# Kernel tuning notes

Hardware: AMD Instinct MI355X
Metric: run time of the kernel (lower is better)

The kernel has to match this reference:

```python
import jax, jax.numpy as jnp
import numpy as np

NEG_INF = -1e6

def setup_inputs() -> dict:
    key = jax.random.key(0)
    ks = jax.random.split(key, 7)
    B, Q, K, D, H = 16, 64, 1024, 256, 128
    return {
        "queries": jax.random.normal(ks[0], (B, Q, D), dtype=jnp.float32),
        "keys": jax.random.normal(ks[1], (B, K, D), dtype=jnp.float32),
        "values": jax.random.normal(ks[2], (B, K, D), dtype=jnp.float32),
        "valid_lens": jax.random.randint(ks[3], (B,), 1, K + 1, dtype=jnp.int32),
        "W_q": jax.random.normal(ks[4], (D, H), dtype=jnp.float32) * (1.0 / np.sqrt(D)),
        "W_k": jax.random.normal(ks[5], (D, H), dtype=jnp.float32) * (1.0 / np.sqrt(D)),
        "w_v": jax.random.normal(ks[6], (H,), dtype=jnp.float32) * (1.0 / np.sqrt(H)),
    }

def reference(queries, keys, values, valid_lens, W_q, W_k, w_v):
    # project: [B,Q,H], [B,K,H]
    q = jnp.einsum('bqd,dh->bqh', queries, W_q)
    k = jnp.einsum('bkd,dh->bkh', keys, W_k)
    # broadcast add -> tanh -> score: [B,Q,K]
    features = jnp.tanh(q[:, :, None, :] + k[:, None, :, :])  # [B,Q,K,H]
    scores = jnp.einsum('bqkh,h->bqk', features, w_v)
    # masked softmax over key axis (valid_lens per batch)
    K_len = keys.shape[1]
    mask = jnp.arange(K_len)[None, None, :] < valid_lens[:, None, None]  # [B,1,K]
    scores = jnp.where(mask, scores, NEG_INF)
    attn = jax.nn.softmax(scores, axis=-1)
    # weighted sum of values: [B,Q,Dv]  (dropout p=0 -> identity)
    return jnp.einsum('bqk,bkd->bqd', attn, values)
```

## Files before the change

### kernel.cpp

```cpp
#include <hip/hip_runtime.h>

#define DDIM 256
#define HDIM 128
#define KLEN 1024
#define SCL 2.8853900817779268f

__global__ __launch_bounds__(256) void proj_kernel(
    const float* __restrict__ queries, const float* __restrict__ keys,
    const float* __restrict__ W_q, const float* __restrict__ W_k,
    float* __restrict__ Eq, float* __restrict__ Ek)
{
    __shared__ union {
        float a[64 * 64];
        float t[32][68];
    } sm;

    const int tid  = threadIdx.x;
    const int lane = tid & 63;
    const int wav  = tid >> 6;

    int blk = blockIdx.x;
    bool iskey; int b = 0, kc0 = 0, hb, row0;
    const float* in; const float* W;
    if (blk < 1024) {
        iskey = true;
        int xcd = blk & 7, s = blk >> 3;
        b = ((s >> 6) << 3) | xcd;
        int r6 = s & 63;
        kc0 = (r6 >> 2) << 6;
        hb  = (r6 & 3) << 5;
        row0 = b * KLEN + kc0;
        in = keys; W = W_k;
    } else {
        iskey = false;
        int qrb = blk - 1024;
        row0 = (qrb >> 2) << 6;
        hb   = (qrb & 3) << 5;
        in = queries; W = W_q;
    }

    const int hg8 = __builtin_amdgcn_readfirstlane(wav << 3);
    const float* Wu = W + hb + hg8;

    const int srow = tid >> 4;
    const int sgd  = tid & 15;
    const float* gsrc = in + (size_t)(row0 + srow) * DDIM + (sgd << 2);

    float4 pf0 = *(const float4*)(gsrc);
    float4 pf1 = *(const float4*)(gsrc + 16 * DDIM);
    float4 pf2 = *(const float4*)(gsrc + 32 * DDIM);
    float4 pf3 = *(const float4*)(gsrc + 48 * DDIM);

    float acc[8];
    #pragma unroll
    for (int c = 0; c < 8; c++) acc[c] = 0.f;

    const int w0 = (srow)      * 64 + ((sgd ^ ((srow)      & 7)) << 2);
    const int w1 = (srow + 16) * 64 + ((sgd ^ ((srow + 16) & 7)) << 2);
    const int w2 = (srow + 32) * 64 + ((sgd ^ ((srow + 32) & 7)) << 2);
    const int w3 = (srow + 48) * 64 + ((sgd ^ ((srow + 48) & 7)) << 2);

    for (int dt0 = 0; dt0 < DDIM; dt0 += 64) {
        *(float4*)(sm.a + w0) = pf0;
        *(float4*)(sm.a + w1) = pf1;
        *(float4*)(sm.a + w2) = pf2;
        *(float4*)(sm.a + w3) = pf3;
        __syncthreads();
        if (dt0 < DDIM - 64) {
            const float* g2 = gsrc + dt0 + 64;
            pf0 = *(const float4*)(g2);
            pf1 = *(const float4*)(g2 + 16 * DDIM);
            pf2 = *(const float4*)(g2 + 32 * DDIM);
            pf3 = *(const float4*)(g2 + 48 * DDIM);
        }
        const float* arow = sm.a + lane * 64;
        const int lx = lane & 7;
        #pragma unroll
        for (int d4 = 0; d4 < 64; d4 += 4) {
            float4 a = *(const float4*)(arow + ((((d4 >> 2)) ^ lx) << 2));
            const float* wr = Wu + (size_t)(dt0 + d4) * HDIM;
            #pragma unroll
            for (int c = 0; c < 8; c++) acc[c] = fmaf(a.x, wr[c],            acc[c]);
            #pragma unroll
            for (int c = 0; c < 8; c++) acc[c] = fmaf(a.y, wr[HDIM + c],     acc[c]);
            #pragma unroll
            for (int c = 0; c < 8; c++) acc[c] = fmaf(a.z, wr[2 * HDIM + c], acc[c]);
            #pragma unroll
            for (int c = 0; c < 8; c++) acc[c] = fmaf(a.w, wr[3 * HDIM + c], acc[c]);
        }
        __syncthreads();
    }

    float e[8];
    #pragma unroll
    for (int c = 0; c < 8; c++) e[c] = __builtin_amdgcn_exp2f(SCL * acc[c]);

    if (!iskey) {
        float* dst = Eq + (size_t)(row0 + lane) * HDIM + hb + hg8;
        *(float4*)(dst)     = make_float4(e[0], e[1], e[2], e[3]);
        *(float4*)(dst + 4) = make_float4(e[4], e[5], e[6], e[7]);
    } else {
        #pragma unroll
        for (int c = 0; c < 8; c++) sm.t[(wav << 3) + c][lane] = e[c];
        __syncthreads();
        float* dstb = Ek + (size_t)b * HDIM * KLEN + (size_t)hb * KLEN + kc0;
        #pragma unroll
        for (int i = 0; i < 2; i++) {
            int g = tid + (i << 8);
            int h = g >> 4, k4 = (g & 15) << 2;
            float4 o = *(const float4*)(&sm.t[h][k4]);
            *(float4*)(dstb + (size_t)h * KLEN + k4) = o;
        }
    }
}

__global__ __launch_bounds__(512) void score_kernel(
    const float* __restrict__ Eq, const float* __restrict__ Ek,
    const float* __restrict__ w_v, const int* __restrict__ valid_lens,
    float* __restrict__ p)
{
    __shared__ float4 eqw[HDIM];
    __shared__ float red0[8], red1[8];

    int tid = threadIdx.x, lane = tid & 63, wav = tid >> 6;
    int blk = blockIdx.x;
    int xcd = blk & 7, s = blk >> 3;
    int b = ((s >= 32) ? 8 : 0) + xcd;
    int qp = s & 31;
    int bq0 = b * 64 + qp * 2;
    int vlen = valid_lens[b];

    if (tid < HDIM) {
        float w2 = -2.0f * w_v[tid];
        eqw[tid] = make_float4(Eq[(size_t)bq0 * HDIM + tid],
                               Eq[(size_t)(bq0 + 1) * HDIM + tid], w2, 0.f);
    }
    __syncthreads();

    int k0 = tid << 1;
    float s00 = -1e30f, s01 = -1e30f, s10 = -1e30f, s11 = -1e30f;
    if (k0 < vlen) {
        const float* ekp = Ek + (size_t)b * HDIM * KLEN + k0;
        float a00 = 0.f, a01 = 0.f, a10 = 0.f, a11 = 0.f;
        #pragma unroll 4
        for (int h = 0; h < HDIM; h++) {
            float2 ek = *(const float2*)(ekp + (size_t)h * KLEN);
            float4 e  = eqw[h];
            a00 = fmaf(e.z, __builtin_amdgcn_rcpf(fmaf(e.x, ek.x, 1.f)), a00);
            a01 = fmaf(e.z, __builtin_amdgcn_rcpf(fmaf(e.x, ek.y, 1.f)), a01);
            a10 = fmaf(e.z, __builtin_amdgcn_rcpf(fmaf(e.y, ek.x, 1.f)), a10);
            a11 = fmaf(e.z, __builtin_amdgcn_rcpf(fmaf(e.y, ek.y, 1.f)), a11);
        }
        s00 = a00; s10 = a10;
        if (k0 + 1 < vlen) { s01 = a01; s11 = a11; }
    }

    float m0 = fmaxf(s00, s01), m1 = fmaxf(s10, s11);
    #pragma unroll
    for (int off = 32; off > 0; off >>= 1) {
        m0 = fmaxf(m0, __shfl_xor(m0, off, 64));
        m1 = fmaxf(m1, __shfl_xor(m1, off, 64));
    }
    if (lane == 0) { red0[wav] = m0; red1[wav] = m1; }
    __syncthreads();
    m0 = red0[0]; m1 = red1[0];
    #pragma unroll
    for (int i = 1; i < 8; i++) {
        m0 = fmaxf(m0, red0[i]);
        m1 = fmaxf(m1, red1[i]);
    }

    float e00 = __expf(s00 - m0), e01 = __expf(s01 - m0);
    float e10 = __expf(s10 - m1), e11 = __expf(s11 - m1);
    float t0 = e00 + e01, t1 = e10 + e11;
    #pragma unroll
    for (int off = 32; off > 0; off >>= 1) {
        t0 += __shfl_xor(t0, off, 64);
        t1 += __shfl_xor(t1, off, 64);
    }
    __syncthreads();
    if (lane == 0) { red0[wav] = t0; red1[wav] = t1; }
    __syncthreads();
    t0 = red0[0]; t1 = red1[0];
    #pragma unroll
    for (int i = 1; i < 8; i++) { t0 += red0[i]; t1 += red1[i]; }
    float inv0 = 1.0f / t0, inv1 = 1.0f / t1;

    float* p0 = p + (size_t)bq0 * KLEN + k0;
    *(float2*)(p0)        = make_float2(e00 * inv0, e01 * inv0);
    *(float2*)(p0 + KLEN) = make_float2(e10 * inv1, e11 * inv1);
}

__global__ __launch_bounds__(256) void av_kernel(
    const float* __restrict__ p, const float* __restrict__ values,
    const int* __restrict__ valid_lens, float* __restrict__ part)
{
    __shared__ float pt[128][10];

    int blk = blockIdx.x;
    int xcd = blk & 7, s = blk >> 3;
    int b = ((s >> 6) << 3) | xcd;
    int r = s & 63, qt = r >> 3, kq = r & 7;
    int tid = threadIdx.x, lane = tid & 63, w = tid >> 6;
    int vlen = valid_lens[b];
    int kbeg = kq << 7;
    int kc = vlen - kbeg; kc = kc < 0 ? 0 : (kc > 128 ? 128 : kc);
    int kc4 = (kc + 3) & ~3;
    int bq0 = b * 64 + qt * 8;

    {
        int q = tid >> 5, k4 = (tid & 31) << 2;
        float4 pv = *(const float4*)(p + (size_t)(bq0 + q) * KLEN + kbeg + k4);
        pt[k4 + 0][q] = pv.x;
        pt[k4 + 1][q] = pv.y;
        pt[k4 + 2][q] = pv.z;
        pt[k4 + 3][q] = pv.w;
    }
    __syncthreads();

    const float* vb = values + ((size_t)b * KLEN + kbeg) * DDIM + (lane << 2);
    float4 a0 = make_float4(0.f, 0.f, 0.f, 0.f);
    float4 a1 = make_float4(0.f, 0.f, 0.f, 0.f);

    for (int k = 0; k < kc4; k += 4) {
        #pragma unroll
        for (int i = 0; i < 4; i++) {
            float2 pp = *(const float2*)(&pt[k + i][w << 1]);
            float4 v  = *(const float4*)(vb + (size_t)(k + i) * DDIM);
            a0.x = fmaf(pp.x, v.x, a0.x); a0.y = fmaf(pp.x, v.y, a0.y);
            a0.z = fmaf(pp.x, v.z, a0.z); a0.w = fmaf(pp.x, v.w, a0.w);
            a1.x = fmaf(pp.y, v.x, a1.x); a1.y = fmaf(pp.y, v.y, a1.y);
            a1.z = fmaf(pp.y, v.z, a1.z); a1.w = fmaf(pp.y, v.w, a1.w);
        }
    }
    float* d0 = part + ((size_t)kq * 1024 + bq0 + (w << 1)) * DDIM + (lane << 2);
    *(float4*)(d0)        = a0;
    *(float4*)(d0 + DDIM) = a1;
}

__global__ __launch_bounds__(256) void combine_kernel(
    const float* __restrict__ part, float* __restrict__ out)
{
    int i = blockIdx.x * 256 + threadIdx.x;
    const float4* p4 = (const float4*)part;
    float4 a = p4[i];
    #pragma unroll
    for (int j = 1; j < 8; j++) {
        float4 v = p4[(size_t)j * 65536 + i];
        a.x += v.x; a.y += v.y; a.z += v.z; a.w += v.w;
    }
    ((float4*)out)[i] = a;
}

extern "C" void kernel_launch(void* const* d_in, const int* in_sizes, int n_in,
                              void* d_out, int out_size, void* d_ws, size_t ws_size,
                              hipStream_t stream) {
    const float* queries    = (const float*)d_in[0];
    const float* keys       = (const float*)d_in[1];
    const float* values     = (const float*)d_in[2];
    const int*   valid_lens = (const int*)d_in[3];
    const float* W_q        = (const float*)d_in[4];
    const float* W_k        = (const float*)d_in[5];
    const float* w_v        = (const float*)d_in[6];

    float* Eq   = (float*)d_ws;
    float* Ek   = Eq + 131072;
    float* p    = Ek + 2097152;
    float* part = Ek;

    proj_kernel<<<1088, 256, 0, stream>>>(queries, keys, W_q, W_k, Eq, Ek);
    score_kernel<<<512, 512, 0, stream>>>(Eq, Ek, w_v, valid_lens, p);
    av_kernel<<<1024, 256, 0, stream>>>(p, values, valid_lens, part);
    combine_kernel<<<256, 256, 0, stream>>>(part, (float*)d_out);
}
```

Measured before the change: 147.5 us.

## Restructure AV kernel so each thread accumulates all eight queries with in-block k reduction

The attention-times-values kernel now has each wave cover a 128-key slice and accumulate all 8 queries of the tile per thread. Each value load is therefore reused across 8 queries instead of 2, and the four waves' partials are reduced in shared memory. The split over keys drops from 8 chunks to 2, so the partial buffer and the combine kernel read a quarter as much data. The grid shrinks to 256 blocks and each thread holds 32 accumulator registers, which may lower occupancy and parallelism on this GPU.

```diff
diff --git a/kernel.cpp b/kernel.cpp
--- a/kernel.cpp
+++ b/kernel.cpp
@@ -195,47 +195,74 @@
     const float* __restrict__ p, const float* __restrict__ values,
     const int* __restrict__ valid_lens, float* __restrict__ part)
 {
-    __shared__ float pt[128][10];
+    __shared__ union {
+        float  pt[512][8];
+        float4 slab[4][8][64];
+    } sm;
 
     int blk = blockIdx.x;
     int xcd = blk & 7, s = blk >> 3;
-    int b = ((s >> 6) << 3) | xcd;
-    int r = s & 63, qt = r >> 3, kq = r & 7;
+    int b = ((s >> 4) << 3) | xcd;
+    int r = s & 15, qt = r >> 1, kh = r & 1;
     int tid = threadIdx.x, lane = tid & 63, w = tid >> 6;
     int vlen = valid_lens[b];
-    int kbeg = kq << 7;
-    int kc = vlen - kbeg; kc = kc < 0 ? 0 : (kc > 128 ? 128 : kc);
-    int kc4 = (kc + 3) & ~3;
     int bq0 = b * 64 + qt * 8;
-
-    {
-        int q = tid >> 5, k4 = (tid & 31) << 2;
-        float4 pv = *(const float4*)(p + (size_t)(bq0 + q) * KLEN + kbeg + k4);
-        pt[k4 + 0][q] = pv.x;
-        pt[k4 + 1][q] = pv.y;
-        pt[k4 + 2][q] = pv.z;
-        pt[k4 + 3][q] = pv.w;
-    }
-    __syncthreads();
-
-    const float* vb = values + ((size_t)b * KLEN + kbeg) * DDIM + (lane << 2);
-    float4 a0 = make_float4(0.f, 0.f, 0.f, 0.f);
-    float4 a1 = make_float4(0.f, 0.f, 0.f, 0.f);
-
-    for (int k = 0; k < kc4; k += 4) {
-        #pragma unroll
-        for (int i = 0; i < 4; i++) {
-            float2 pp = *(const float2*)(&pt[k + i][w << 1]);
-            float4 v  = *(const float4*)(vb + (size_t)(k + i) * DDIM);
-            a0.x = fmaf(pp.x, v.x, a0.x); a0.y = fmaf(pp.x, v.y, a0.y);
-            a0.z = fmaf(pp.x, v.z, a0.z); a0.w = fmaf(pp.x, v.w, a0.w);
-            a1.x = fmaf(pp.y, v.x, a1.x); a1.y = fmaf(pp.y, v.y, a1.y);
-            a1.z = fmaf(pp.y, v.z, a1.z); a1.w = fmaf(pp.y, v.w, a1.w);
-        }
-    }
-    float* d0 = part + ((size_t)kq * 1024 + bq0 + (w << 1)) * DDIM + (lane << 2);
-    *(float4*)(d0)        = a0;
-    *(float4*)(d0 + DDIM) = a1;
+    int kbase = kh << 9;
+
+    #pragma unroll
+    for (int i = 0; i < 4; i++) {
+        int slot = tid + (i << 8);
+        int q = slot >> 7, k4 = (slot & 127) << 2;
+        float4 pv = *(const float4*)(p + (size_t)(bq0 + q) * KLEN + kbase + k4);
+        sm.pt[k4 + 0][q] = pv.x;
+        sm.pt[k4 + 1][q] = pv.y;
+        sm.pt[k4 + 2][q] = pv.z;
+        sm.pt[k4 + 3][q] = pv.w;
+    }
+    __syncthreads();
+
+    int kw = w << 7;
+    int cnt = vlen - (kbase + kw); cnt = cnt < 0 ? 0 : (cnt > 128 ? 128 : cnt);
+    int cnt4 = (cnt + 3) & ~3;
+    const float* vb = values + ((size_t)b * KLEN + kbase + kw) * DDIM + (lane << 2);
+
+    float4 acc[8];
+    #pragma unroll
+    for (int q = 0; q < 8; q++) acc[q] = make_float4(0.f, 0.f, 0.f, 0.f);
+
+    for (int k = 0; k < cnt4; k += 4) {
+        #pragma unroll
+        for (int j = 0; j < 4; j++) {
+            float4 v  = *(const float4*)(vb + (size_t)(k + j) * DDIM);
+            float4 p0 = *(const float4*)(&sm.pt[kw + k + j][0]);
+            float4 p1 = *(const float4*)(&sm.pt[kw + k + j][4]);
+            float pq[8] = {p0.x, p0.y, p0.z, p0.w, p1.x, p1.y, p1.z, p1.w};
+            #pragma unroll
+            for (int q = 0; q < 8; q++) {
+                acc[q].x = fmaf(pq[q], v.x, acc[q].x);
+                acc[q].y = fmaf(pq[q], v.y, acc[q].y);
+                acc[q].z = fmaf(pq[q], v.z, acc[q].z);
+                acc[q].w = fmaf(pq[q], v.w, acc[q].w);
+            }
+        }
+    }
+
+    __syncthreads();
+    #pragma unroll
+    for (int q = 0; q < 8; q++) sm.slab[w][q][lane] = acc[q];
+    __syncthreads();
+    #pragma unroll
+    for (int e = 0; e < 2; e++) {
+        int slot = (tid << 1) | e;
+        int q = slot >> 6, d4 = slot & 63;
+        float4 a = sm.slab[0][q][d4];
+        #pragma unroll
+        for (int g = 1; g < 4; g++) {
+            float4 t = sm.slab[g][q][d4];
+            a.x += t.x; a.y += t.y; a.z += t.z; a.w += t.w;
+        }
+        *(float4*)(part + ((size_t)kh * 1024 + bq0 + q) * DDIM + (d4 << 2)) = a;
+    }
 }
 
 __global__ __launch_bounds__(256) void combine_kernel(
@@ -244,11 +271,8 @@
     int i = blockIdx.x * 256 + threadIdx.x;
     const float4* p4 = (const float4*)part;
     float4 a = p4[i];
-    #pragma unroll
-    for (int j = 1; j < 8; j++) {
-        float4 v = p4[(size_t)j * 65536 + i];
-        a.x += v.x; a.y += v.y; a.z += v.z; a.w += v.w;
-    }
+    float4 v = p4[65536 + i];
+    a.x += v.x; a.y += v.y; a.z += v.z; a.w += v.w;
     ((float4*)out)[i] = a;
 }
 
@@ -270,6 +294,6 @@
 
     proj_kernel<<<1088, 256, 0, stream>>>(queries, keys, W_q, W_k, Eq, Ek);
     score_kernel<<<512, 512, 0, stream>>>(Eq, Ek, w_v, valid_lens, p);
-    av_kernel<<<1024, 256, 0, stream>>>(p, values, valid_lens, part);
+    av_kernel<<<256, 256, 0, stream>>>(p, values, valid_lens, part);
     combine_kernel<<<256, 256, 0, stream>>>(part, (float*)d_out);
 }
```

After: 147.1 us. Within noise of the previous version (-0.3%).
